# Optimization experiments

Hardware: AMD Instinct MI355X
Metric: run time of the kernel (lower is better)

Reference implementation:

```python
import jax, jax.numpy as jnp
import numpy as np

LABEL_SMOOTHING = 0.1
K_SLOPE = 5.0
N, D = 8192, 256


def setup_inputs() -> dict:
    key = jax.random.key(0)
    k1, k2, k3 = jax.random.split(key, 3)
    return {
        "image_features1": jax.random.normal(k1, (N, D), dtype=jnp.float32),
        "image_features2": jax.random.normal(k2, (N, D), dtype=jnp.float32),
        "logit_scale": jnp.asarray(14.2857, dtype=jnp.float32),  # ~ 1/0.07 CLIP temp
        "positive_weights": jax.random.normal(k3, (N,), dtype=jnp.float32),
    }


def _l2_normalize(x, axis=-1, eps=1e-12):
    # matches F.normalize(dim=-1)
    norm = jnp.linalg.norm(x, axis=axis, keepdims=True)
    return x / jnp.maximum(norm, eps)


def _weighted_infonce(sim, eps):
    # per row i: (1-eps_i)*(-sim[i,i] + lse_i) + eps_i*(-mean(sim[i,:]) + lse_i)
    #          = lse_i - (1-eps_i)*sim[i,i] - eps_i*mean_i
    n = sim.shape[0]
    lse = jax.nn.logsumexp(sim, axis=1)            # [n]
    diag = jnp.diagonal(sim)                       # [n]
    row_mean = jnp.mean(sim, axis=1)               # [n]
    per_row = lse - (1.0 - eps) * diag - eps * row_mean
    return jnp.sum(per_row) / n


def reference(image_features1, image_features2, logit_scale, positive_weights):
    f1 = _l2_normalize(image_features1)
    f2 = _l2_normalize(image_features2)
    logits12 = logit_scale * (f1 @ f2.T)           # [N, N]
    # eps = 1 - (1 - label_smoothing) * sigmoid(k * w)
    eps = 1.0 - (1.0 - LABEL_SMOOTHING) * jax.nn.sigmoid(K_SLOPE * positive_weights)
    loss1 = _weighted_infonce(logits12, eps)
    loss2 = _weighted_infonce(logits12.T, eps)
    return (loss1 + loss2) / 2.0
```

## Files before the change

### kernel.cpp

```cpp
#include <hip/hip_runtime.h>
#include <hip/hip_bf16.h>

#define NN 8192
#define DD 256
#define LOG2E 1.4426950408889634f
#define LN2f 0.6931471805599453f

typedef __attribute__((ext_vector_type(8))) short short8;
typedef __attribute__((ext_vector_type(4))) float f32x4;

__device__ __forceinline__ unsigned short f2bf(float x) {
    unsigned int u = __float_as_uint(x);
    u += 0x7fff + ((u >> 16) & 1);
    return (unsigned short)(u >> 16);
}
__device__ __forceinline__ float epsf(float w) {
    return 1.f - 0.9f / (1.f + __expf(-5.f * w));
}

__global__ __launch_bounds__(256) void nrm_kernel(
    const float* __restrict__ f1, const float* __restrict__ f2,
    const float* __restrict__ scale_p, const float* __restrict__ wts,
    unsigned short* __restrict__ f1n, unsigned short* __restrict__ f2n,
    float* __restrict__ diag, float* __restrict__ rse, float* __restrict__ cse,
    float* __restrict__ S1p, float* __restrict__ S2p,
    float* __restrict__ T1p, float* __restrict__ T2p)
{
    __shared__ float4 red[4][256];
    const int w = threadIdx.x >> 6, lane = threadIdx.x & 63;
    const int row = blockIdx.x * 4 + w;
    const float4 a = reinterpret_cast<const float4*>(f1 + (size_t)row * DD)[lane];
    const float4 b = reinterpret_cast<const float4*>(f2 + (size_t)row * DD)[lane];
    float sa = a.x * a.x + a.y * a.y + a.z * a.z + a.w * a.w;
    float sb = b.x * b.x + b.y * b.y + b.z * b.z + b.w * b.w;
    float sab = a.x * b.x + a.y * b.y + a.z * b.z + a.w * b.w;
#pragma unroll
    for (int off = 1; off < 64; off <<= 1) {
        sa += __shfl_xor(sa, off);
        sb += __shfl_xor(sb, off);
        sab += __shfl_xor(sab, off);
    }
    const float s = scale_p[0];
    const float n1 = fmaxf(sqrtf(sa), 1e-12f);
    const float n2 = fmaxf(sqrtf(sb), 1e-12f);
    const float e = epsf(wts[row]);
    if (lane == 0) { diag[row] = s * sab / (n1 * n2); rse[row] = 0.f; cse[row] = 0.f; }
    const float r1 = s * LOG2E / n1, r2 = 1.0f / n2;
    const float v0 = a.x * r1, v1 = a.y * r1, v2 = a.z * r1, v3 = a.w * r1;
    const float u0 = b.x * r2, u1 = b.y * r2, u2 = b.z * r2, u3 = b.w * r2;
    ushort4 o1, o2;
    o1.x = f2bf(v0); o1.y = f2bf(v1); o1.z = f2bf(v2); o1.w = f2bf(v3);
    o2.x = f2bf(u0); o2.y = f2bf(u1); o2.z = f2bf(u2); o2.w = f2bf(u3);
    reinterpret_cast<ushort4*>(f1n + (size_t)row * DD)[lane] = o1;
    reinterpret_cast<ushort4*>(f2n + (size_t)row * DD)[lane] = o2;
    red[w][lane * 4 + 0] = make_float4(v0, e * v0, u0, e * u0);
    red[w][lane * 4 + 1] = make_float4(v1, e * v1, u1, e * u1);
    red[w][lane * 4 + 2] = make_float4(v2, e * v2, u2, e * u2);
    red[w][lane * 4 + 3] = make_float4(v3, e * v3, u3, e * u3);
    __syncthreads();
    const int c = threadIdx.x;
    const int part = (blockIdx.x & 63) * 256 + c;
    const float4 q0 = red[0][c], q1 = red[1][c], q2 = red[2][c], q3 = red[3][c];
    atomicAdd(&S1p[part], q0.x + q1.x + q2.x + q3.x);
    atomicAdd(&T1p[part], q0.y + q1.y + q2.y + q3.y);
    atomicAdd(&S2p[part], q0.z + q1.z + q2.z + q3.z);
    atomicAdd(&T2p[part], q0.w + q1.w + q2.w + q3.w);
}

__global__ __launch_bounds__(256, 2) void gemm_kernel(
    const unsigned short* __restrict__ f1n, const unsigned short* __restrict__ f2n,
    float* __restrict__ rowsumexp, float* __restrict__ colsumexp)
{
    __shared__ char Bs[4][32 * 512];
    __shared__ float colbuf[2][1024];
    const int bid = blockIdx.x;
    const int bm = bid >> 3, bc = bid & 7;
    const int w = threadIdx.x >> 6, lane = threadIdx.x & 63;
    const int wr = (w >> 1) * 64, wc = (w & 1) * 16;
    const int lhi = lane >> 4, llo = lane & 15;

    const char* aBase = (const char*)f1n + ((size_t)(bm * 128 + wr + llo) * 512) + lhi * 16;
    short8 av[4][8];
#pragma unroll
    for (int m = 0; m < 4; ++m)
#pragma unroll
        for (int ks = 0; ks < 8; ++ks)
            av[m][ks] = *(const short8*)(aBase + (size_t)(m * 16) * 512 + ks * 64);
#pragma unroll
    for (int m = 0; m < 4; ++m)
#pragma unroll
        for (int ks = 0; ks < 8; ++ks)
            asm volatile("" : "+v"(av[m][ks]));

    const char* bBase = (const char*)f2n + (size_t)bc * 1024 * 512;

    auto stage = [&](int tile) {
        char* dst = Bs[tile & 3] + (w * 8) * 512;
        const char* src = bBase + (size_t)(tile * 32) * 512;
#pragma unroll
        for (int i = 0; i < 4; ++i) {
            const int r = w * 8 + i * 2 + (lane >> 5);
            const int cs = (lane & 31) ^ (r & 15);
            __builtin_amdgcn_global_load_lds(
                (const __attribute__((address_space(1))) unsigned int*)(src + (size_t)r * 512 + cs * 16),
                (__attribute__((address_space(3))) unsigned int*)(dst + i * 2 * 512), 16, 0, 0);
        }
    };

    float rowpart[16];
#pragma unroll
    for (int i = 0; i < 16; ++i) rowpart[i] = 0.f;

    const int rb = wc + llo;
    const int sw = llo << 4;

    auto body = [&](int t) {
        const char* bs = Bs[t & 3];
        f32x4 acc[4];
#pragma unroll
        for (int m = 0; m < 4; ++m) acc[m] = (f32x4){0.f, 0.f, 0.f, 0.f};
        __builtin_amdgcn_s_setprio(1);
#pragma unroll
        for (int ks = 0; ks < 8; ++ks) {
            const int kb = ks * 64 + lhi * 16;
            const short8 bv = *(const short8*)(bs + rb * 512 + (kb ^ sw));
#pragma unroll
            for (int m = 0; m < 4; ++m)
                acc[m] = __builtin_amdgcn_mfma_f32_16x16x32_bf16(av[m][ks], bv, acc[m], 0, 0, 0);
        }
        __builtin_amdgcn_s_setprio(0);
        float cee = 0.f;
#pragma unroll
        for (int m = 0; m < 4; ++m)
#pragma unroll
            for (int j = 0; j < 4; ++j) {
                const float e = __builtin_exp2f(acc[m][j]);
                rowpart[m * 4 + j] += e;
                cee += e;
            }
        cee += __shfl_xor(cee, 16); cee += __shfl_xor(cee, 32);
        if (lhi == 0) colbuf[w >> 1][t * 32 + wc + llo] = cee;
    };

    stage(0); stage(1); stage(2);

    for (int t = 0; t < 29; ++t) {
        asm volatile("s_waitcnt vmcnt(8)" ::: "memory");
        __builtin_amdgcn_s_barrier();
        asm volatile("" ::: "memory");
        __builtin_amdgcn_sched_barrier(0);
        stage(t + 3);
        body(t);
    }
    asm volatile("s_waitcnt vmcnt(8)" ::: "memory");
    __builtin_amdgcn_s_barrier();
    asm volatile("" ::: "memory");
    __builtin_amdgcn_sched_barrier(0);
    body(29);
    asm volatile("s_waitcnt vmcnt(4)" ::: "memory");
    __builtin_amdgcn_s_barrier();
    asm volatile("" ::: "memory");
    __builtin_amdgcn_sched_barrier(0);
    body(30);
    asm volatile("s_waitcnt vmcnt(0)" ::: "memory");
    __builtin_amdgcn_s_barrier();
    asm volatile("" ::: "memory");
    __builtin_amdgcn_sched_barrier(0);
    body(31);

    __syncthreads();
#pragma unroll
    for (int m = 0; m < 4; ++m)
#pragma unroll
        for (int j = 0; j < 4; ++j) {
            float v = rowpart[m * 4 + j];
            v += __shfl_xor(v, 1); v += __shfl_xor(v, 2);
            v += __shfl_xor(v, 4); v += __shfl_xor(v, 8);
            if (llo == 0)
                atomicAdd(&rowsumexp[bm * 128 + wr + m * 16 + lhi * 4 + j], v);
        }
    for (int c = threadIdx.x; c < 1024; c += 256)
        atomicAdd(&colsumexp[bc * 1024 + c], colbuf[0][c] + colbuf[1][c]);
}

__global__ __launch_bounds__(1024) void fin_kernel(
    const float* __restrict__ rse, const float* __restrict__ cse,
    const float* __restrict__ diag, const float* __restrict__ wts,
    const float* __restrict__ S1p, const float* __restrict__ S2p,
    const float* __restrict__ T1p, const float* __restrict__ T2p,
    float* __restrict__ out)
{
    const int t = threadIdx.x;
    float a = 0.f;
#pragma unroll
    for (int k = 0; k < 8; ++k) {
        const int i = t + k * 1024;
        a += __logf(rse[i]) + __logf(cse[i]) - 2.f * (1.f - epsf(wts[i])) * diag[i];
    }
    if (t < 256) {
        float s1 = 0.f, t1 = 0.f, s2 = 0.f, t2 = 0.f;
        for (int p = 0; p < 64; ++p) {
            const int idx = p * 256 + t;
            s1 += S1p[idx]; t1 += T1p[idx]; s2 += S2p[idx]; t2 += T2p[idx];
        }
        a -= (t1 * s2 + s1 * t2) * (LN2f / (float)NN);
    }
#pragma unroll
    for (int off = 1; off < 64; off <<= 1) a += __shfl_xor(a, off);
    __shared__ float red[16];
    if ((t & 63) == 0) red[t >> 6] = a;
    __syncthreads();
    if (t == 0) {
        float tot = 0.f;
#pragma unroll
        for (int i = 0; i < 16; ++i) tot += red[i];
        out[0] = tot * (1.f / (2.f * (float)NN));
    }
}

extern "C" void kernel_launch(void* const* d_in, const int* in_sizes, int n_in,
                              void* d_out, int out_size, void* d_ws, size_t ws_size,
                              hipStream_t stream) {
    (void)in_sizes; (void)n_in; (void)out_size; (void)ws_size;
    const float* f1 = (const float*)d_in[0];
    const float* f2 = (const float*)d_in[1];
    const float* scale = (const float*)d_in[2];
    const float* wts = (const float*)d_in[3];
    float* out = (float*)d_out;

    char* ws = (char*)d_ws;
    unsigned short* f1n = (unsigned short*)ws;
    unsigned short* f2n = (unsigned short*)(ws + (size_t)4 * 1024 * 1024);
    float* fb = (float*)(ws + (size_t)8 * 1024 * 1024);
    float* rse  = fb;
    float* cse  = fb + 8192;
    float* diag = fb + 16384;
    float* S1p  = fb + 24576;
    float* S2p  = fb + 24576 + 16384;
    float* T1p  = fb + 24576 + 32768;
    float* T2p  = fb + 24576 + 49152;

    hipMemsetAsync(S1p, 0, (size_t)4 * 16384 * sizeof(float), stream);
    nrm_kernel<<<NN / 4, 256, 0, stream>>>(f1, f2, scale, wts, f1n, f2n,
                                           diag, rse, cse, S1p, S2p, T1p, T2p);
    gemm_kernel<<<512, 256, 0, stream>>>(f1n, f2n, rse, cse);
    fin_kernel<<<1, 1024, 0, stream>>>(rse, cse, diag, wts, S1p, S2p, T1p, T2p, out);
}
```

Measured before the change: 80.03 us.

## Load B tiles directly into registers instead of LDS-staged pipeline

The GEMM kernel drops the 4-deep LDS ring buffer, which was filled with global_load_lds and guarded by barriers. Each wave now loads its own 16-column slice of f2n straight into registers and double-buffers it, so the warps split columns 512 each instead of sharing tiles. This removes LDS traffic and per-tile barriers, but each wave now reads B separately, with less data reuse and more register pressure. The final kernel also splits the 64-way partial reduction across all 1024 threads rather than 256.

```diff
diff --git a/kernel.cpp b/kernel.cpp
--- a/kernel.cpp
+++ b/kernel.cpp
@@ -71,15 +71,15 @@
     const unsigned short* __restrict__ f1n, const unsigned short* __restrict__ f2n,
     float* __restrict__ rowsumexp, float* __restrict__ colsumexp)
 {
-    __shared__ char Bs[4][32 * 512];
     __shared__ float colbuf[2][1024];
     const int bid = blockIdx.x;
     const int bm = bid >> 3, bc = bid & 7;
     const int w = threadIdx.x >> 6, lane = threadIdx.x & 63;
-    const int wr = (w >> 1) * 64, wc = (w & 1) * 16;
+    const int wh = w >> 1;
+    const int wch = (w & 1) * 512;
     const int lhi = lane >> 4, llo = lane & 15;
 
-    const char* aBase = (const char*)f1n + ((size_t)(bm * 128 + wr + llo) * 512) + lhi * 16;
+    const char* aBase = (const char*)f1n + ((size_t)(bm * 128 + wh * 64 + llo) * 512) + lhi * 16;
     short8 av[4][8];
 #pragma unroll
     for (int m = 0; m < 4; ++m)
@@ -92,42 +92,29 @@
         for (int ks = 0; ks < 8; ++ks)
             asm volatile("" : "+v"(av[m][ks]));
 
-    const char* bBase = (const char*)f2n + (size_t)bc * 1024 * 512;
-
-    auto stage = [&](int tile) {
-        char* dst = Bs[tile & 3] + (w * 8) * 512;
-        const char* src = bBase + (size_t)(tile * 32) * 512;
-#pragma unroll
-        for (int i = 0; i < 4; ++i) {
-            const int r = w * 8 + i * 2 + (lane >> 5);
-            const int cs = (lane & 31) ^ (r & 15);
-            __builtin_amdgcn_global_load_lds(
-                (const __attribute__((address_space(1))) unsigned int*)(src + (size_t)r * 512 + cs * 16),
-                (__attribute__((address_space(3))) unsigned int*)(dst + i * 2 * 512), 16, 0, 0);
-        }
+    float rowpart[16];
+#pragma unroll
+    for (int i = 0; i < 16; ++i) rowpart[i] = 0.f;
+
+    const char* pB = (const char*)f2n +
+                     (size_t)(bc * 1024 + wch + llo) * 512 + lhi * 16;
+
+    auto loadB = [&](short8 (&P)[8], const char* p) {
+#pragma unroll
+        for (int ks = 0; ks < 8; ++ks)
+            P[ks] = *(const short8*)(p + ks * 64);
     };
 
-    float rowpart[16];
-#pragma unroll
-    for (int i = 0; i < 16; ++i) rowpart[i] = 0.f;
-
-    const int rb = wc + llo;
-    const int sw = llo << 4;
-
-    auto body = [&](int t) {
-        const char* bs = Bs[t & 3];
+    auto computeTile = [&](short8 (&P)[8], int t) {
         f32x4 acc[4];
 #pragma unroll
         for (int m = 0; m < 4; ++m) acc[m] = (f32x4){0.f, 0.f, 0.f, 0.f};
         __builtin_amdgcn_s_setprio(1);
 #pragma unroll
-        for (int ks = 0; ks < 8; ++ks) {
-            const int kb = ks * 64 + lhi * 16;
-            const short8 bv = *(const short8*)(bs + rb * 512 + (kb ^ sw));
+        for (int ks = 0; ks < 8; ++ks)
 #pragma unroll
             for (int m = 0; m < 4; ++m)
-                acc[m] = __builtin_amdgcn_mfma_f32_16x16x32_bf16(av[m][ks], bv, acc[m], 0, 0, 0);
-        }
+                acc[m] = __builtin_amdgcn_mfma_f32_16x16x32_bf16(av[m][ks], P[ks], acc[m], 0, 0, 0);
         __builtin_amdgcn_s_setprio(0);
         float cee = 0.f;
 #pragma unroll
@@ -139,34 +126,19 @@
                 cee += e;
             }
         cee += __shfl_xor(cee, 16); cee += __shfl_xor(cee, 32);
-        if (lhi == 0) colbuf[w >> 1][t * 32 + wc + llo] = cee;
+        if (lhi == 0) colbuf[wh][wch + t * 16 + llo] = cee;
     };
 
-    stage(0); stage(1); stage(2);
-
-    for (int t = 0; t < 29; ++t) {
-        asm volatile("s_waitcnt vmcnt(8)" ::: "memory");
-        __builtin_amdgcn_s_barrier();
-        asm volatile("" ::: "memory");
-        __builtin_amdgcn_sched_barrier(0);
-        stage(t + 3);
-        body(t);
-    }
-    asm volatile("s_waitcnt vmcnt(8)" ::: "memory");
-    __builtin_amdgcn_s_barrier();
-    asm volatile("" ::: "memory");
-    __builtin_amdgcn_sched_barrier(0);
-    body(29);
-    asm volatile("s_waitcnt vmcnt(4)" ::: "memory");
-    __builtin_amdgcn_s_barrier();
-    asm volatile("" ::: "memory");
-    __builtin_amdgcn_sched_barrier(0);
-    body(30);
-    asm volatile("s_waitcnt vmcnt(0)" ::: "memory");
-    __builtin_amdgcn_s_barrier();
-    asm volatile("" ::: "memory");
-    __builtin_amdgcn_sched_barrier(0);
-    body(31);
+    short8 p0[8], p1[8];
+    loadB(p0, pB);
+#pragma unroll
+    for (int tp = 0; tp < 16; ++tp) {
+        loadB(p1, pB + 8192);
+        computeTile(p0, 2 * tp);
+        if (tp < 15) loadB(p0, pB + 16384);
+        computeTile(p1, 2 * tp + 1);
+        pB += 16384;
+    }
 
     __syncthreads();
 #pragma unroll
@@ -177,7 +149,7 @@
             v += __shfl_xor(v, 1); v += __shfl_xor(v, 2);
             v += __shfl_xor(v, 4); v += __shfl_xor(v, 8);
             if (llo == 0)
-                atomicAdd(&rowsumexp[bm * 128 + wr + m * 16 + lhi * 4 + j], v);
+                atomicAdd(&rowsumexp[bm * 128 + wh * 64 + m * 16 + lhi * 4 + j], v);
         }
     for (int c = threadIdx.x; c < 1024; c += 256)
         atomicAdd(&colsumexp[bc * 1024 + c], colbuf[0][c] + colbuf[1][c]);
@@ -197,12 +169,24 @@
         const int i = t + k * 1024;
         a += __logf(rse[i]) + __logf(cse[i]) - 2.f * (1.f - epsf(wts[i])) * diag[i];
     }
-    if (t < 256) {
+    __shared__ float4 pr4[4][256];
+    {
+        const int col = t & 255, seg = t >> 8;
         float s1 = 0.f, t1 = 0.f, s2 = 0.f, t2 = 0.f;
-        for (int p = 0; p < 64; ++p) {
-            const int idx = p * 256 + t;
+#pragma unroll
+        for (int q = 0; q < 16; ++q) {
+            const int idx = (seg * 16 + q) * 256 + col;
             s1 += S1p[idx]; t1 += T1p[idx]; s2 += S2p[idx]; t2 += T2p[idx];
         }
+        pr4[seg][col] = make_float4(s1, t1, s2, t2);
+    }
+    __syncthreads();
+    if (t < 256) {
+        const float4 q0 = pr4[0][t], q1 = pr4[1][t], q2 = pr4[2][t], q3 = pr4[3][t];
+        const float s1 = q0.x + q1.x + q2.x + q3.x;
+        const float t1 = q0.y + q1.y + q2.y + q3.y;
+        const float s2 = q0.z + q1.z + q2.z + q3.z;
+        const float t2 = q0.w + q1.w + q2.w + q3.w;
         a -= (t1 * s2 + s1 * t2) * (LN2f / (float)NN);
     }
 #pragma unroll
```

After: 252.7 us. 216% more time.
